# Performance work log

Hardware: AMD Instinct MI355X
Metric: run time of the kernel (lower is better)

Reference implementation:

```python
import jax, jax.numpy as jnp
import numpy as np

N_ATOMS = 131072
AEV_DIM = 1008
OUT_DIM = 2  # sum(predicted_dim) == len(predicted_properties)
ALPHA = 0.1  # CELU alpha (ANI standard)
# per-element hidden widths for ['H','C','O','N','S','F','Cl']
WIDTHS = [(256, 192, 160), (224, 192, 160), (192, 160, 128), (192, 160, 128),
          (160, 128, 96), (160, 128, 96), (160, 128, 96)]
W1MAX, W2MAX, W3MAX = 256, 192, 160


def _celu(x):
    return jax.nn.celu(x, alpha=ALPHA)


def setup_inputs() -> dict:
    key = jax.random.key(0)
    ks = jax.random.split(key, 2 + 7 * 8)
    species = jax.random.randint(ks[0], (N_ATOMS,), 0, 7)
    aev = jax.random.normal(ks[1], (N_ATOMS, AEV_DIM), dtype=jnp.float32)

    # Padded, stacked per-element weights; only the [:w] blocks are used.
    W1 = np.zeros((7, AEV_DIM, W1MAX), np.float32); b1 = np.zeros((7, W1MAX), np.float32)
    W2 = np.zeros((7, W1MAX, W2MAX), np.float32);  b2 = np.zeros((7, W2MAX), np.float32)
    W3 = np.zeros((7, W2MAX, W3MAX), np.float32);  b3 = np.zeros((7, W3MAX), np.float32)
    Wh = np.zeros((7, W3MAX, OUT_DIM), np.float32); bh = np.zeros((7, OUT_DIM), np.float32)
    for e, (w1, w2, w3) in enumerate(WIDTHS):
        kk = ks[2 + 8 * e: 2 + 8 * (e + 1)]
        W1[e, :, :w1] = np.asarray(jax.random.normal(kk[0], (AEV_DIM, w1))) / np.sqrt(AEV_DIM)
        b1[e, :w1] = np.asarray(jax.random.normal(kk[1], (w1,))) * 0.01
        W2[e, :w1, :w2] = np.asarray(jax.random.normal(kk[2], (w1, w2))) / np.sqrt(w1)
        b2[e, :w2] = np.asarray(jax.random.normal(kk[3], (w2,))) * 0.01
        W3[e, :w2, :w3] = np.asarray(jax.random.normal(kk[4], (w2, w3))) / np.sqrt(w2)
        b3[e, :w3] = np.asarray(jax.random.normal(kk[5], (w3,))) * 0.01
        Wh[e, :w3, :] = np.asarray(jax.random.normal(kk[6], (w3, OUT_DIM))) / np.sqrt(w3)
        bh[e, :] = np.asarray(jax.random.normal(kk[7], (OUT_DIM,))) * 0.01
    return {
        "species": species, "aev": aev,
        "W1": jnp.asarray(W1), "b1": jnp.asarray(b1),
        "W2": jnp.asarray(W2), "b2": jnp.asarray(b2),
        "W3": jnp.asarray(W3), "b3": jnp.asarray(b3),
        "Wh": jnp.asarray(Wh), "bh": jnp.asarray(bh),
    }


def reference(species, aev, W1, b1, W2, b2, W3, b3, Wh, bh):
    # species-routed dispatch -> per-element 3-layer MLP + 2 linear heads -> combine
    out = jnp.zeros((aev.shape[0], OUT_DIM), dtype=aev.dtype)
    for e, (w1, w2, w3) in enumerate(WIDTHS):  # fixed set of 7 structurally distinct experts
        h = _celu(aev @ W1[e, :, :w1] + b1[e, :w1])          # [N, w1]
        h = _celu(h @ W2[e, :w1, :w2] + b2[e, :w2])          # [N, w2]
        h = _celu(h @ W3[e, :w2, :w3] + b3[e, :w3])          # [N, w3]
        y = h @ Wh[e, :w3, :] + bh[e]                        # [N, 2]
        out = out + jnp.where((species == e)[:, None], y, jnp.zeros((), aev.dtype))
    return out
```

## Files before the change

kernel.cpp:

```cpp
#include <hip/hip_runtime.h>

#define NS 7
#define NA 131072
#define AEVD 1008
#define KP1 1024
#define N1 256
#define N2 192
#define N3 160

typedef __attribute__((ext_vector_type(8))) short short8;
typedef __attribute__((ext_vector_type(8))) unsigned short ushortx8;
typedef __attribute__((ext_vector_type(4))) float f32x4;
typedef __attribute__((ext_vector_type(4))) float fvec4;
typedef unsigned short u16;

#define BAR() asm volatile("s_waitcnt lgkmcnt(0)\ns_barrier" ::: "memory")

__device__ __forceinline__ u16 f2bf(float f) {
  unsigned u = __builtin_bit_cast(unsigned, f);
  u += 0x7fffu + ((u >> 16) & 1u);
  return (u16)(u >> 16);
}
__device__ __forceinline__ float bf2f(u16 h) {
  return __builtin_bit_cast(float, ((unsigned)h) << 16);
}
__device__ __forceinline__ float celu_f(float x) {
  return x > 0.f ? x : 0.1f * (__expf(x * 10.f) - 1.f);
}
__device__ __forceinline__ void pack8(fvec4 a, fvec4 b, ushortx8* dst) {
  ushortx8 p;
  p[0] = f2bf(a.x); p[1] = f2bf(a.y); p[2] = f2bf(a.z); p[3] = f2bf(a.w);
  p[4] = f2bf(b.x); p[5] = f2bf(b.y); p[6] = f2bf(b.z); p[7] = f2bf(b.w);
  *dst = p;
}
__device__ __forceinline__ fvec4 ld_aev(const float* row, int k) {
  if (k < AEVD) return *(const fvec4*)(row + k);
  fvec4 z = {0.f, 0.f, 0.f, 0.f};
  return z;
}

__global__ void count_kernel(const int* __restrict__ species, int* __restrict__ counts) {
  __shared__ int h[NS];
  if (threadIdx.x < NS) h[threadIdx.x] = 0;
  __syncthreads();
  int i = blockIdx.x * blockDim.x + threadIdx.x;
  if (i < NA) atomicAdd(&h[species[i]], 1);
  __syncthreads();
  if (threadIdx.x < NS) atomicAdd(&counts[threadIdx.x], h[threadIdx.x]);
}

__global__ void scan_kernel(const int* __restrict__ counts, int* __restrict__ offsets,
                            int* __restrict__ cursors, int* __restrict__ blockStart) {
  int off = 0, bs = 0;
  for (int e = 0; e < NS; ++e) {
    offsets[e] = off; cursors[e] = off; blockStart[e] = bs;
    off += counts[e];
    bs += (counts[e] + 63) >> 6;
  }
  offsets[NS] = off; blockStart[NS] = bs;
}

__global__ void scatter_kernel(const int* __restrict__ species, int* __restrict__ cursors,
                               int* __restrict__ idx) {
  __shared__ int h[NS], lb[NS];
  if (threadIdx.x < NS) h[threadIdx.x] = 0;
  __syncthreads();
  int i = blockIdx.x * blockDim.x + threadIdx.x;
  int s = species[i];
  int lpos = atomicAdd(&h[s], 1);
  __syncthreads();
  if (threadIdx.x < NS) lb[threadIdx.x] = atomicAdd(&cursors[threadIdx.x], h[threadIdx.x]);
  __syncthreads();
  idx[lb[s] + lpos] = i;
}

__global__ void convert_w(const float* __restrict__ src, u16* __restrict__ dst,
                          int K, int N, int KP) {
  long total = (long)NS * N * KP;
  for (long i = (long)blockIdx.x * blockDim.x + threadIdx.x; i < total;
       i += (long)gridDim.x * blockDim.x) {
    int kp = (int)(i % KP);
    long t2 = i / KP;
    int n = (int)(t2 % N);
    int e = (int)(t2 / N);
    float v = (kp < K) ? src[((long)e * K + kp) * N + n] : 0.f;
    dst[i] = f2bf(v);
  }
}

#define H1P 264
#define H2P 200
#define H3P 168

__global__ __launch_bounds__(256, 2) void ani_fused(
    const int* __restrict__ idx, const int* __restrict__ counts,
    const int* __restrict__ offsets, const int* __restrict__ blockStart,
    const float* __restrict__ aev,
    const u16* __restrict__ W1t, const float* __restrict__ b1,
    const u16* __restrict__ W2t, const float* __restrict__ b2,
    const u16* __restrict__ W3t, const float* __restrict__ b3,
    const u16* __restrict__ Wht, const float* __restrict__ bh,
    float* __restrict__ out) {
  __shared__ __align__(16) u16 AB[2][64 * 72];
  __shared__ __align__(16) u16 H1[64 * H1P];
  __shared__ __align__(16) u16 H2[64 * H2P];
  u16* H3 = H1;

  int bid = blockIdx.x;
  if (bid >= blockStart[NS]) return;
  int e = 0;
#pragma unroll
  for (int s = 1; s < NS; ++s)
    if (bid >= blockStart[s]) e = s;
  int t = bid - blockStart[e];
  int base = offsets[e] + (t << 6);
  int mcount = counts[e] - (t << 6);
  if (mcount > 64) mcount = 64;

  int tid = threadIdx.x;
  int lane = tid & 63;
  int w = tid >> 6;
  int lr = lane & 15;
  int kg = lane >> 4;

  int arow = tid >> 2;
  int aks = (tid & 3) << 4;
  int rrow = arow < mcount ? arow : (mcount - 1);
  const float* aevRow = aev + (size_t)idx[base + rrow] * AEVD;

  const u16* Wb1 = W1t + ((size_t)e * N1 + (w * 64 + lr)) * KP1 + kg * 8;

  auto loadA = [&](int chunk, fvec4 (&v)[4]) {
    int kb = chunk * 64 + aks;
    v[0] = ld_aev(aevRow, kb);
    v[1] = ld_aev(aevRow, kb + 4);
    v[2] = ld_aev(aevRow, kb + 8);
    v[3] = ld_aev(aevRow, kb + 12);
  };
  auto loadB1 = [&](int chunk, short8 (&b)[2][4]) {
#pragma unroll
    for (int kk = 0; kk < 2; ++kk)
#pragma unroll
      for (int ni = 0; ni < 4; ++ni)
        b[kk][ni] = *(const short8*)(Wb1 + (size_t)ni * 16 * KP1 + chunk * 64 + kk * 32);
  };

  f32x4 acc[4][4] = {};

  auto iter1 = [&](int c, int p, short8 (&bfr)[2][4], fvec4 (&pre)[4]) {
    short8 af[2][4];
#pragma unroll
    for (int kk = 0; kk < 2; ++kk)
#pragma unroll
      for (int mi = 0; mi < 4; ++mi)
        af[kk][mi] = *(const short8*)&AB[p][(mi * 16 + lr) * 72 + kk * 32 + kg * 8];
    if (c + 1 < 16) {
      pack8(pre[0], pre[1], (ushortx8*)&AB[p ^ 1][arow * 72 + aks]);
      pack8(pre[2], pre[3], (ushortx8*)&AB[p ^ 1][arow * 72 + aks + 8]);
    }
    if (c + 3 < 16) loadA(c + 3, pre);
#pragma unroll
    for (int kk = 0; kk < 2; ++kk)
#pragma unroll
      for (int ni = 0; ni < 4; ++ni)
#pragma unroll
        for (int mi = 0; mi < 4; ++mi)
          acc[mi][ni] = __builtin_amdgcn_mfma_f32_16x16x32_bf16(af[kk][mi], bfr[kk][ni], acc[mi][ni], 0, 0, 0);
    if (c + 2 < 16) loadB1(c + 2, bfr);
    BAR();
  };

  {
    fvec4 t0[4];
    loadA(0, t0);
    pack8(t0[0], t0[1], (ushortx8*)&AB[0][arow * 72 + aks]);
    pack8(t0[2], t0[3], (ushortx8*)&AB[0][arow * 72 + aks + 8]);
  }
  fvec4 pA[4], pB[4];
  loadA(1, pA);
  loadA(2, pB);
  short8 bA[2][4], bB[2][4];
  loadB1(0, bA);
  loadB1(1, bB);
  BAR();

  for (int c = 0; c < 16; c += 2) {
    iter1(c, 0, bA, pA);
    iter1(c + 1, 1, bB, pB);
  }

  int mr2 = (w & 1) * 32;
  int nc2 = (w >> 1) * 96;
  const u16* Wb2 = W2t + ((size_t)e * N2 + (nc2 + lr)) * N1 + kg * 8;
  auto loadB2 = [&](int k0, short8 (&b)[6]) {
#pragma unroll
    for (int ni = 0; ni < 6; ++ni)
      b[ni] = *(const short8*)(Wb2 + (size_t)ni * 16 * N1 + k0);
  };
  short8 c2A[6], c2B[6], c2C[6], c2D[6];
  loadB2(0, c2A); loadB2(32, c2B); loadB2(64, c2C); loadB2(96, c2D);

#pragma unroll
  for (int ni = 0; ni < 4; ++ni) {
    int col = w * 64 + ni * 16 + lr;
    float bias = b1[e * N1 + col];
#pragma unroll
    for (int mi = 0; mi < 4; ++mi)
#pragma unroll
      for (int r = 0; r < 4; ++r)
        H1[(mi * 16 + kg * 4 + r) * H1P + col] = f2bf(celu_f(acc[mi][ni][r] + bias));
  }
  BAR();

  f32x4 acc2[2][6] = {};
  auto mm2 = [&](int k0, short8 (&b)[6]) {
    short8 a0 = *(const short8*)&H1[(mr2 + lr) * H1P + k0 + kg * 8];
    short8 a1 = *(const short8*)&H1[(mr2 + 16 + lr) * H1P + k0 + kg * 8];
#pragma unroll
    for (int ni = 0; ni < 6; ++ni) {
      acc2[0][ni] = __builtin_amdgcn_mfma_f32_16x16x32_bf16(a0, b[ni], acc2[0][ni], 0, 0, 0);
      acc2[1][ni] = __builtin_amdgcn_mfma_f32_16x16x32_bf16(a1, b[ni], acc2[1][ni], 0, 0, 0);
    }
  };
  mm2(0, c2A);   loadB2(128, c2A);
  mm2(32, c2B);  loadB2(160, c2B);
  mm2(64, c2C);  loadB2(192, c2C);
  mm2(96, c2D);  loadB2(224, c2D);
  mm2(128, c2A);
  mm2(160, c2B);
  mm2(192, c2C);
  mm2(224, c2D);

  int mr3 = (w & 1) * 32;
  int nc3 = (w >> 1) * 80;
  const u16* Wb3 = W3t + ((size_t)e * N3 + (nc3 + lr)) * N2 + kg * 8;
  auto loadB3 = [&](int k0, short8 (&b)[5]) {
#pragma unroll
    for (int ni = 0; ni < 5; ++ni)
      b[ni] = *(const short8*)(Wb3 + (size_t)ni * 16 * N2 + k0);
  };
  short8 c3A[5], c3B[5], c3C[5];
  loadB3(0, c3A); loadB3(32, c3B); loadB3(64, c3C);

#pragma unroll
  for (int ni = 0; ni < 6; ++ni) {
    int col = nc2 + ni * 16 + lr;
    float bias = b2[e * N2 + col];
#pragma unroll
    for (int mi = 0; mi < 2; ++mi)
#pragma unroll
      for (int r = 0; r < 4; ++r)
        H2[(mr2 + mi * 16 + kg * 4 + r) * H2P + col] = f2bf(celu_f(acc2[mi][ni][r] + bias));
  }
  BAR();

  f32x4 acc3[2][5] = {};
  auto mm3 = [&](int k0, short8 (&b)[5]) {
    short8 a0 = *(const short8*)&H2[(mr3 + lr) * H2P + k0 + kg * 8];
    short8 a1 = *(const short8*)&H2[(mr3 + 16 + lr) * H2P + k0 + kg * 8];
#pragma unroll
    for (int ni = 0; ni < 5; ++ni) {
      acc3[0][ni] = __builtin_amdgcn_mfma_f32_16x16x32_bf16(a0, b[ni], acc3[0][ni], 0, 0, 0);
      acc3[1][ni] = __builtin_amdgcn_mfma_f32_16x16x32_bf16(a1, b[ni], acc3[1][ni], 0, 0, 0);
    }
  };
  mm3(0, c3A);   loadB3(96, c3A);
  mm3(32, c3B);  loadB3(128, c3B);
  mm3(64, c3C);  loadB3(160, c3C);
  mm3(96, c3A);
  mm3(128, c3B);
  mm3(160, c3C);

  int hr_ = tid >> 2;
  int ho = (tid >> 1) & 1;
  int kh = tid & 1;
  const u16* wr = Wht + ((size_t)e * 2 + ho) * N3 + kh * 80;
  ushortx8 wvv[10];
#pragma unroll
  for (int c = 0; c < 10; ++c) wvv[c] = *(const ushortx8*)&wr[c * 8];

#pragma unroll
  for (int ni = 0; ni < 5; ++ni) {
    int col = nc3 + ni * 16 + lr;
    float bias = b3[e * N3 + col];
#pragma unroll
    for (int mi = 0; mi < 2; ++mi)
#pragma unroll
      for (int r = 0; r < 4; ++r)
        H3[(mr3 + mi * 16 + kg * 4 + r) * H3P + col] = f2bf(celu_f(acc3[mi][ni][r] + bias));
  }
  BAR();

  {
    float s = 0.f;
    const u16* hrow = &H3[hr_ * H3P + kh * 80];
#pragma unroll
    for (int c = 0; c < 10; ++c) {
      ushortx8 hv = *(const ushortx8*)&hrow[c * 8];
#pragma unroll
      for (int j = 0; j < 8; ++j) s += bf2f(hv[j]) * bf2f(wvv[c][j]);
    }
    s += __shfl_xor(s, 1);
    if (kh == 0 && hr_ < mcount) out[(size_t)idx[base + hr_] * 2 + ho] = s + bh[e * 2 + ho];
  }
}

extern "C" void kernel_launch(void* const* d_in, const int* in_sizes, int n_in,
                              void* d_out, int out_size, void* d_ws, size_t ws_size,
                              hipStream_t stream) {
  const int* species = (const int*)d_in[0];
  const float* aev = (const float*)d_in[1];
  const float* W1 = (const float*)d_in[2];
  const float* b1 = (const float*)d_in[3];
  const float* W2 = (const float*)d_in[4];
  const float* b2 = (const float*)d_in[5];
  const float* W3 = (const float*)d_in[6];
  const float* b3 = (const float*)d_in[7];
  const float* Wh = (const float*)d_in[8];
  const float* bh = (const float*)d_in[9];
  float* out = (float*)d_out;

  char* p = (char*)d_ws;
  int* counts = (int*)p; p += 32;
  int* offsets = (int*)p; p += 32;
  int* cursors = (int*)p; p += 32;
  int* blockStart = (int*)p; p += 32;
  int* idx = (int*)p; p += (size_t)NA * 4;
  u16* W1t = (u16*)p; p += (size_t)NS * N1 * KP1 * 2;
  u16* W2t = (u16*)p; p += (size_t)NS * N2 * N1 * 2;
  u16* W3t = (u16*)p; p += (size_t)NS * N3 * N2 * 2;
  u16* Wht = (u16*)p; p += (size_t)NS * 2 * N3 * 2;

  (void)hipMemsetAsync(counts, 0, 32, stream);
  count_kernel<<<NA / 256, 256, 0, stream>>>(species, counts);
  scan_kernel<<<1, 1, 0, stream>>>(counts, offsets, cursors, blockStart);
  scatter_kernel<<<NA / 256, 256, 0, stream>>>(species, cursors, idx);

  convert_w<<<2048, 256, 0, stream>>>(W1, W1t, AEVD, N1, KP1);
  convert_w<<<1024, 256, 0, stream>>>(W2, W2t, N1, N2, N1);
  convert_w<<<512, 256, 0, stream>>>(W3, W3t, N2, N3, N2);
  convert_w<<<16, 256, 0, stream>>>(Wh, Wht, N3, 2, N3);

  int maxBlocks = (NA >> 6) + NS;
  ani_fused<<<maxBlocks, 256, 0, stream>>>(idx, counts, offsets, blockStart, aev,
                                           W1t, b1, W2t, b2, W3t, b3, Wht, bh, out);
}
```

Before: 328.5 us.

## Restructure layer-1 GEMM into four 256-wide K quarters with deep register prefetch

Measured after the change: 358.9 us. 1.09x slower.

```diff
diff --git a/kernel.cpp b/kernel.cpp
--- a/kernel.cpp
+++ b/kernel.cpp
@@ -10,11 +10,10 @@
 
 typedef __attribute__((ext_vector_type(8))) short short8;
 typedef __attribute__((ext_vector_type(8))) unsigned short ushortx8;
+typedef __attribute__((ext_vector_type(4))) unsigned short ushortx4;
 typedef __attribute__((ext_vector_type(4))) float f32x4;
 typedef __attribute__((ext_vector_type(4))) float fvec4;
 typedef unsigned short u16;
-
-#define BAR() asm volatile("s_waitcnt lgkmcnt(0)\ns_barrier" ::: "memory")
 
 __device__ __forceinline__ u16 f2bf(float f) {
   unsigned u = __builtin_bit_cast(unsigned, f);
@@ -26,17 +25,6 @@
 }
 __device__ __forceinline__ float celu_f(float x) {
   return x > 0.f ? x : 0.1f * (__expf(x * 10.f) - 1.f);
-}
-__device__ __forceinline__ void pack8(fvec4 a, fvec4 b, ushortx8* dst) {
-  ushortx8 p;
-  p[0] = f2bf(a.x); p[1] = f2bf(a.y); p[2] = f2bf(a.z); p[3] = f2bf(a.w);
-  p[4] = f2bf(b.x); p[5] = f2bf(b.y); p[6] = f2bf(b.z); p[7] = f2bf(b.w);
-  *dst = p;
-}
-__device__ __forceinline__ fvec4 ld_aev(const float* row, int k) {
-  if (k < AEVD) return *(const fvec4*)(row + k);
-  fvec4 z = {0.f, 0.f, 0.f, 0.f};
-  return z;
 }
 
 __global__ void count_kernel(const int* __restrict__ species, int* __restrict__ counts) {
@@ -88,7 +76,7 @@
   }
 }
 
-#define H1P 264
+#define AP 264
 #define H2P 200
 #define H3P 168
 
@@ -101,10 +89,10 @@
     const u16* __restrict__ W3t, const float* __restrict__ b3,
     const u16* __restrict__ Wht, const float* __restrict__ bh,
     float* __restrict__ out) {
-  __shared__ __align__(16) u16 AB[2][64 * 72];
-  __shared__ __align__(16) u16 H1[64 * H1P];
-  __shared__ __align__(16) u16 H2[64 * H2P];
-  u16* H3 = H1;
+  __shared__ __align__(16) u16 S[2][64 * AP];
+  u16* H1 = &S[0][0];
+  u16* H2 = &S[1][0];
+  u16* H3 = &S[0][0];
 
   int bid = blockIdx.x;
   if (bid >= blockStart[NS]) return;
@@ -124,70 +112,59 @@
   int kg = lane >> 4;
 
   int arow = tid >> 2;
-  int aks = (tid & 3) << 4;
+  int sub = tid & 3;
   int rrow = arow < mcount ? arow : (mcount - 1);
   const float* aevRow = aev + (size_t)idx[base + rrow] * AEVD;
 
   const u16* Wb1 = W1t + ((size_t)e * N1 + (w * 64 + lr)) * KP1 + kg * 8;
 
-  auto loadA = [&](int chunk, fvec4 (&v)[4]) {
-    int kb = chunk * 64 + aks;
-    v[0] = ld_aev(aevRow, kb);
-    v[1] = ld_aev(aevRow, kb + 4);
-    v[2] = ld_aev(aevRow, kb + 8);
-    v[3] = ld_aev(aevRow, kb + 12);
-  };
-  auto loadB1 = [&](int chunk, short8 (&b)[2][4]) {
-#pragma unroll
-    for (int kk = 0; kk < 2; ++kk)
+  fvec4 L[16];
+  auto loadQ = [&](int q) {
+#pragma unroll
+    for (int j = 0; j < 16; ++j) {
+      int k = q * 256 + (sub + j * 4) * 4;
+      if (k < AEVD) L[j] = *(const fvec4*)(aevRow + k);
+      else { fvec4 z = {0.f, 0.f, 0.f, 0.f}; L[j] = z; }
+    }
+  };
+  auto packQ = [&](int b) {
+#pragma unroll
+    for (int j = 0; j < 16; ++j) {
+      ushortx4 p;
+      p[0] = f2bf(L[j].x); p[1] = f2bf(L[j].y);
+      p[2] = f2bf(L[j].z); p[3] = f2bf(L[j].w);
+      *(ushortx4*)&S[b][arow * AP + (sub + j * 4) * 4] = p;
+    }
+  };
+
+  f32x4 acc[4][4] = {};
+  auto computeQ = [&](int q, int b) {
+#pragma unroll
+    for (int ks = 0; ks < 8; ++ks) {
+      short8 af[4], bf[4];
+#pragma unroll
+      for (int mi = 0; mi < 4; ++mi)
+        af[mi] = *(const short8*)&S[b][(mi * 16 + lr) * AP + ks * 32 + kg * 8];
 #pragma unroll
       for (int ni = 0; ni < 4; ++ni)
-        b[kk][ni] = *(const short8*)(Wb1 + (size_t)ni * 16 * KP1 + chunk * 64 + kk * 32);
-  };
-
-  f32x4 acc[4][4] = {};
-
-  auto iter1 = [&](int c, int p, short8 (&bfr)[2][4], fvec4 (&pre)[4]) {
-    short8 af[2][4];
-#pragma unroll
-    for (int kk = 0; kk < 2; ++kk)
-#pragma unroll
-      for (int mi = 0; mi < 4; ++mi)
-        af[kk][mi] = *(const short8*)&AB[p][(mi * 16 + lr) * 72 + kk * 32 + kg * 8];
-    if (c + 1 < 16) {
-      pack8(pre[0], pre[1], (ushortx8*)&AB[p ^ 1][arow * 72 + aks]);
-      pack8(pre[2], pre[3], (ushortx8*)&AB[p ^ 1][arow * 72 + aks + 8]);
-    }
-    if (c + 3 < 16) loadA(c + 3, pre);
-#pragma unroll
-    for (int kk = 0; kk < 2; ++kk)
+        bf[ni] = *(const short8*)(Wb1 + (size_t)ni * 16 * KP1 + q * 256 + ks * 32);
 #pragma unroll
       for (int ni = 0; ni < 4; ++ni)
 #pragma unroll
         for (int mi = 0; mi < 4; ++mi)
-          acc[mi][ni] = __builtin_amdgcn_mfma_f32_16x16x32_bf16(af[kk][mi], bfr[kk][ni], acc[mi][ni], 0, 0, 0);
-    if (c + 2 < 16) loadB1(c + 2, bfr);
-    BAR();
-  };
-
-  {
-    fvec4 t0[4];
-    loadA(0, t0);
-    pack8(t0[0], t0[1], (ushortx8*)&AB[0][arow * 72 + aks]);
-    pack8(t0[2], t0[3], (ushortx8*)&AB[0][arow * 72 + aks + 8]);
-  }
-  fvec4 pA[4], pB[4];
-  loadA(1, pA);
-  loadA(2, pB);
-  short8 bA[2][4], bB[2][4];
-  loadB1(0, bA);
-  loadB1(1, bB);
-  BAR();
-
-  for (int c = 0; c < 16; c += 2) {
-    iter1(c, 0, bA, pA);
-    iter1(c + 1, 1, bB, pB);
-  }
+          acc[mi][ni] = __builtin_amdgcn_mfma_f32_16x16x32_bf16(af[mi], bf[ni], acc[mi][ni], 0, 0, 0);
+    }
+  };
+
+  loadQ(0); packQ(0); loadQ(1);
+  __syncthreads();
+  computeQ(0, 0); packQ(1); loadQ(2);
+  __syncthreads();
+  computeQ(1, 1); packQ(0); loadQ(3);
+  __syncthreads();
+  computeQ(2, 0); packQ(1);
+  __syncthreads();
+  computeQ(3, 1);
 
   int mr2 = (w & 1) * 32;
   int nc2 = (w >> 1) * 96;
@@ -208,14 +185,14 @@
     for (int mi = 0; mi < 4; ++mi)
 #pragma unroll
       for (int r = 0; r < 4; ++r)
-        H1[(mi * 16 + kg * 4 + r) * H1P + col] = f2bf(celu_f(acc[mi][ni][r] + bias));
-  }
-  BAR();
+        H1[(mi * 16 + kg * 4 + r) * AP + col] = f2bf(celu_f(acc[mi][ni][r] + bias));
+  }
+  __syncthreads();
 
   f32x4 acc2[2][6] = {};
   auto mm2 = [&](int k0, short8 (&b)[6]) {
-    short8 a0 = *(const short8*)&H1[(mr2 + lr) * H1P + k0 + kg * 8];
-    short8 a1 = *(const short8*)&H1[(mr2 + 16 + lr) * H1P + k0 + kg * 8];
+    short8 a0 = *(const short8*)&H1[(mr2 + lr) * AP + k0 + kg * 8];
+    short8 a1 = *(const short8*)&H1[(mr2 + 16 + lr) * AP + k0 + kg * 8];
 #pragma unroll
     for (int ni = 0; ni < 6; ++ni) {
       acc2[0][ni] = __builtin_amdgcn_mfma_f32_16x16x32_bf16(a0, b[ni], acc2[0][ni], 0, 0, 0);
@@ -252,7 +229,7 @@
       for (int r = 0; r < 4; ++r)
         H2[(mr2 + mi * 16 + kg * 4 + r) * H2P + col] = f2bf(celu_f(acc2[mi][ni][r] + bias));
   }
-  BAR();
+  __syncthreads();
 
   f32x4 acc3[2][5] = {};
   auto mm3 = [&](int k0, short8 (&b)[5]) {
@@ -289,7 +266,7 @@
       for (int r = 0; r < 4; ++r)
         H3[(mr3 + mi * 16 + kg * 4 + r) * H3P + col] = f2bf(celu_f(acc3[mi][ni][r] + bias));
   }
-  BAR();
+  __syncthreads();
 
   {
     float s = 0.f;
```

## Shrink tiles to 32 atoms with 2 waves, remap blocks across XCDs

Applied to the files above, without the earlier changes.

Measured after the change: 428.7 us. 30.5% more time.

```diff
diff --git a/kernel.cpp b/kernel.cpp
--- a/kernel.cpp
+++ b/kernel.cpp
@@ -7,6 +7,11 @@
 #define N1 256
 #define N2 192
 #define N3 160
+#define GR 32
+#define APITCH 40
+#define H1P 264
+#define H2P 200
+#define H3P 168
 
 typedef __attribute__((ext_vector_type(8))) short short8;
 typedef __attribute__((ext_vector_type(8))) unsigned short ushortx8;
@@ -27,14 +32,8 @@
 __device__ __forceinline__ float celu_f(float x) {
   return x > 0.f ? x : 0.1f * (__expf(x * 10.f) - 1.f);
 }
-__device__ __forceinline__ void pack8(fvec4 a, fvec4 b, ushortx8* dst) {
-  ushortx8 p;
-  p[0] = f2bf(a.x); p[1] = f2bf(a.y); p[2] = f2bf(a.z); p[3] = f2bf(a.w);
-  p[4] = f2bf(b.x); p[5] = f2bf(b.y); p[6] = f2bf(b.z); p[7] = f2bf(b.w);
-  *dst = p;
-}
 __device__ __forceinline__ fvec4 ld_aev(const float* row, int k) {
-  if (k < AEVD) return *(const fvec4*)(row + k);
+  if (k + 4 <= AEVD) return *(const fvec4*)(row + k);
   fvec4 z = {0.f, 0.f, 0.f, 0.f};
   return z;
 }
@@ -50,14 +49,14 @@
 }
 
 __global__ void scan_kernel(const int* __restrict__ counts, int* __restrict__ offsets,
-                            int* __restrict__ cursors, int* __restrict__ blockStart) {
-  int off = 0, bs = 0;
+                            int* __restrict__ cursors, int* __restrict__ gstart) {
+  int off = 0, gs = 0;
   for (int e = 0; e < NS; ++e) {
-    offsets[e] = off; cursors[e] = off; blockStart[e] = bs;
+    offsets[e] = off; cursors[e] = off; gstart[e] = gs;
     off += counts[e];
-    bs += (counts[e] + 63) >> 6;
-  }
-  offsets[NS] = off; blockStart[NS] = bs;
+    gs += (counts[e] + GR - 1) / GR;
+  }
+  offsets[NS] = off; gstart[NS] = gs;
 }
 
 __global__ void scatter_kernel(const int* __restrict__ species, int* __restrict__ cursors,
@@ -88,34 +87,36 @@
   }
 }
 
-#define H1P 264
-#define H2P 200
-#define H3P 168
-
-__global__ __launch_bounds__(256, 2) void ani_fused(
+__global__ __launch_bounds__(128, 2) void ani_fused(
     const int* __restrict__ idx, const int* __restrict__ counts,
-    const int* __restrict__ offsets, const int* __restrict__ blockStart,
+    const int* __restrict__ offsets, const int* __restrict__ gstart,
     const float* __restrict__ aev,
     const u16* __restrict__ W1t, const float* __restrict__ b1,
     const u16* __restrict__ W2t, const float* __restrict__ b2,
     const u16* __restrict__ W3t, const float* __restrict__ b3,
     const u16* __restrict__ Wht, const float* __restrict__ bh,
     float* __restrict__ out) {
-  __shared__ __align__(16) u16 AB[2][64 * 72];
-  __shared__ __align__(16) u16 H1[64 * H1P];
-  __shared__ __align__(16) u16 H2[64 * H2P];
-  u16* H3 = H1;
-
-  int bid = blockIdx.x;
-  if (bid >= blockStart[NS]) return;
+  __shared__ __align__(16) u16 REG0[GR * H2P];
+  __shared__ __align__(16) u16 REG1[GR * H1P];
+  u16* H1 = REG1;
+  u16* H2 = REG0;
+  u16* H3 = REG1;
+
+  int gd = gridDim.x;
+  int b0 = blockIdx.x;
+  int q = gd >> 3, r = gd & 7;
+  int xcd = b0 & 7, ii = b0 >> 3;
+  int bid = (xcd < r ? xcd * (q + 1) : r * (q + 1) + (xcd - r) * q) + ii;
+
+  if (bid >= gstart[NS]) return;
   int e = 0;
 #pragma unroll
   for (int s = 1; s < NS; ++s)
-    if (bid >= blockStart[s]) e = s;
-  int t = bid - blockStart[e];
-  int base = offsets[e] + (t << 6);
-  int mcount = counts[e] - (t << 6);
-  if (mcount > 64) mcount = 64;
+    if (bid >= gstart[s]) e = s;
+  int t0 = bid - gstart[e];
+  int base = offsets[e] + t0 * GR;
+  int mcount = counts[e] - t0 * GR;
+  if (mcount > GR) mcount = GR;
 
   int tid = threadIdx.x;
   int lane = tid & 63;
@@ -124,152 +125,133 @@
   int kg = lane >> 4;
 
   int arow = tid >> 2;
-  int aks = (tid & 3) << 4;
-  int rrow = arow < mcount ? arow : (mcount - 1);
+  int koff = (tid & 3) << 3;
+  int rrow = arow < mcount ? arow : mcount - 1;
   const float* aevRow = aev + (size_t)idx[base + rrow] * AEVD;
 
-  const u16* Wb1 = W1t + ((size_t)e * N1 + (w * 64 + lr)) * KP1 + kg * 8;
-
-  auto loadA = [&](int chunk, fvec4 (&v)[4]) {
-    int kb = chunk * 64 + aks;
-    v[0] = ld_aev(aevRow, kb);
-    v[1] = ld_aev(aevRow, kb + 4);
-    v[2] = ld_aev(aevRow, kb + 8);
-    v[3] = ld_aev(aevRow, kb + 12);
-  };
-  auto loadB1 = [&](int chunk, short8 (&b)[2][4]) {
-#pragma unroll
-    for (int kk = 0; kk < 2; ++kk)
-#pragma unroll
-      for (int ni = 0; ni < 4; ++ni)
-        b[kk][ni] = *(const short8*)(Wb1 + (size_t)ni * 16 * KP1 + chunk * 64 + kk * 32);
-  };
-
-  f32x4 acc[4][4] = {};
-
-  auto iter1 = [&](int c, int p, short8 (&bfr)[2][4], fvec4 (&pre)[4]) {
-    short8 af[2][4];
-#pragma unroll
-    for (int kk = 0; kk < 2; ++kk)
-#pragma unroll
-      for (int mi = 0; mi < 4; ++mi)
-        af[kk][mi] = *(const short8*)&AB[p][(mi * 16 + lr) * 72 + kk * 32 + kg * 8];
-    if (c + 1 < 16) {
-      pack8(pre[0], pre[1], (ushortx8*)&AB[p ^ 1][arow * 72 + aks]);
-      pack8(pre[2], pre[3], (ushortx8*)&AB[p ^ 1][arow * 72 + aks + 8]);
+  const u16* Wb1 = W1t + ((size_t)e * N1 + (w * 128 + lr)) * KP1 + kg * 8;
+
+  fvec4 Ar[3][2];
+  short8 Br[2][8];
+
+  auto loadA = [&](int c, fvec4 (&d)[2]) {
+    int k = c * 32 + koff;
+    d[0] = ld_aev(aevRow, k);
+    d[1] = ld_aev(aevRow, k + 4);
+  };
+  auto packA = [&](fvec4 (&v)[2], int buf) {
+    ushortx8 p;
+    p[0] = f2bf(v[0].x); p[1] = f2bf(v[0].y); p[2] = f2bf(v[0].z); p[3] = f2bf(v[0].w);
+    p[4] = f2bf(v[1].x); p[5] = f2bf(v[1].y); p[6] = f2bf(v[1].z); p[7] = f2bf(v[1].w);
+    *(ushortx8*)&REG0[buf * GR * APITCH + arow * APITCH + koff] = p;
+  };
+  auto loadB1 = [&](int c, short8 (&d)[8]) {
+#pragma unroll
+    for (int ni = 0; ni < 8; ++ni)
+      d[ni] = *(const short8*)(Wb1 + (size_t)ni * 16 * KP1 + c * 32);
+  };
+
+  f32x4 acc[2][8] = {};
+
+  loadA(0, Ar[0]); loadA(1, Ar[1]); loadA(2, Ar[2]);
+  loadB1(0, Br[0]); loadB1(1, Br[1]);
+  packA(Ar[0], 0);
+  BAR();
+
+#pragma unroll
+  for (int c = 0; c < 32; ++c) {
+    if (c + 3 < 32) loadA(c + 3, Ar[(c + 3) % 3]);
+    short8 af0 = *(const short8*)&REG0[(c & 1) * GR * APITCH + lr * APITCH + kg * 8];
+    short8 af1 = *(const short8*)&REG0[(c & 1) * GR * APITCH + (16 + lr) * APITCH + kg * 8];
+    __builtin_amdgcn_s_setprio(1);
+#pragma unroll
+    for (int ni = 0; ni < 8; ++ni) {
+      acc[0][ni] = __builtin_amdgcn_mfma_f32_16x16x32_bf16(af0, Br[c & 1][ni], acc[0][ni], 0, 0, 0);
+      acc[1][ni] = __builtin_amdgcn_mfma_f32_16x16x32_bf16(af1, Br[c & 1][ni], acc[1][ni], 0, 0, 0);
     }
-    if (c + 3 < 16) loadA(c + 3, pre);
-#pragma unroll
-    for (int kk = 0; kk < 2; ++kk)
-#pragma unroll
-      for (int ni = 0; ni < 4; ++ni)
-#pragma unroll
-        for (int mi = 0; mi < 4; ++mi)
-          acc[mi][ni] = __builtin_amdgcn_mfma_f32_16x16x32_bf16(af[kk][mi], bfr[kk][ni], acc[mi][ni], 0, 0, 0);
-    if (c + 2 < 16) loadB1(c + 2, bfr);
+    __builtin_amdgcn_s_setprio(0);
+    if (c + 1 < 32) packA(Ar[(c + 1) % 3], (c + 1) & 1);
+    if (c + 2 < 32) loadB1(c + 2, Br[c & 1]);
     BAR();
-  };
-
-  {
-    fvec4 t0[4];
-    loadA(0, t0);
-    pack8(t0[0], t0[1], (ushortx8*)&AB[0][arow * 72 + aks]);
-    pack8(t0[2], t0[3], (ushortx8*)&AB[0][arow * 72 + aks + 8]);
-  }
-  fvec4 pA[4], pB[4];
-  loadA(1, pA);
-  loadA(2, pB);
-  short8 bA[2][4], bB[2][4];
-  loadB1(0, bA);
-  loadB1(1, bB);
+  }
+
+  const u16* Wb2 = W2t + ((size_t)e * N2 + (w * 96 + lr)) * N1 + kg * 8;
+  auto loadB2 = [&](int ks, short8 (&d)[6]) {
+#pragma unroll
+    for (int ni = 0; ni < 6; ++ni)
+      d[ni] = *(const short8*)(Wb2 + (size_t)ni * 16 * N1 + ks * 32);
+  };
+  short8 r2a[6], r2b[6];
+  loadB2(0, r2a); loadB2(1, r2b);
+
+#pragma unroll
+  for (int ni = 0; ni < 8; ++ni) {
+    int col = w * 128 + ni * 16 + lr;
+    float bias = b1[e * N1 + col];
+#pragma unroll
+    for (int mi = 0; mi < 2; ++mi)
+#pragma unroll
+      for (int rr = 0; rr < 4; ++rr)
+        H1[(mi * 16 + kg * 4 + rr) * H1P + col] = f2bf(celu_f(acc[mi][ni][rr] + bias));
+  }
   BAR();
 
-  for (int c = 0; c < 16; c += 2) {
-    iter1(c, 0, bA, pA);
-    iter1(c + 1, 1, bB, pB);
-  }
-
-  int mr2 = (w & 1) * 32;
-  int nc2 = (w >> 1) * 96;
-  const u16* Wb2 = W2t + ((size_t)e * N2 + (nc2 + lr)) * N1 + kg * 8;
-  auto loadB2 = [&](int k0, short8 (&b)[6]) {
-#pragma unroll
-    for (int ni = 0; ni < 6; ++ni)
-      b[ni] = *(const short8*)(Wb2 + (size_t)ni * 16 * N1 + k0);
-  };
-  short8 c2A[6], c2B[6], c2C[6], c2D[6];
-  loadB2(0, c2A); loadB2(32, c2B); loadB2(64, c2C); loadB2(96, c2D);
-
-#pragma unroll
-  for (int ni = 0; ni < 4; ++ni) {
-    int col = w * 64 + ni * 16 + lr;
-    float bias = b1[e * N1 + col];
-#pragma unroll
-    for (int mi = 0; mi < 4; ++mi)
-#pragma unroll
-      for (int r = 0; r < 4; ++r)
-        H1[(mi * 16 + kg * 4 + r) * H1P + col] = f2bf(celu_f(acc[mi][ni][r] + bias));
-  }
-  BAR();
-
   f32x4 acc2[2][6] = {};
-  auto mm2 = [&](int k0, short8 (&b)[6]) {
-    short8 a0 = *(const short8*)&H1[(mr2 + lr) * H1P + k0 + kg * 8];
-    short8 a1 = *(const short8*)&H1[(mr2 + 16 + lr) * H1P + k0 + kg * 8];
+  auto mm2 = [&](int ks, short8 (&b)[6]) {
+    short8 a0 = *(const short8*)&H1[lr * H1P + ks * 32 + kg * 8];
+    short8 a1 = *(const short8*)&H1[(16 + lr) * H1P + ks * 32 + kg * 8];
 #pragma unroll
     for (int ni = 0; ni < 6; ++ni) {
       acc2[0][ni] = __builtin_amdgcn_mfma_f32_16x16x32_bf16(a0, b[ni], acc2[0][ni], 0, 0, 0);
       acc2[1][ni] = __builtin_amdgcn_mfma_f32_16x16x32_bf16(a1, b[ni], acc2[1][ni], 0, 0, 0);
     }
   };
-  mm2(0, c2A);   loadB2(128, c2A);
-  mm2(32, c2B);  loadB2(160, c2B);
-  mm2(64, c2C);  loadB2(192, c2C);
-  mm2(96, c2D);  loadB2(224, c2D);
-  mm2(128, c2A);
-  mm2(160, c2B);
-  mm2(192, c2C);
-  mm2(224, c2D);
-
-  int mr3 = (w & 1) * 32;
-  int nc3 = (w >> 1) * 80;
-  const u16* Wb3 = W3t + ((size_t)e * N3 + (nc3 + lr)) * N2 + kg * 8;
-  auto loadB3 = [&](int k0, short8 (&b)[5]) {
+  mm2(0, r2a); loadB2(2, r2a);
+  mm2(1, r2b); loadB2(3, r2b);
+  mm2(2, r2a); loadB2(4, r2a);
+  mm2(3, r2b); loadB2(5, r2b);
+  mm2(4, r2a); loadB2(6, r2a);
+  mm2(5, r2b); loadB2(7, r2b);
+  mm2(6, r2a);
+  mm2(7, r2b);
+
+  const u16* Wb3 = W3t + ((size_t)e * N3 + (w * 80 + lr)) * N2 + kg * 8;
+  auto loadB3 = [&](int ks, short8 (&d)[5]) {
 #pragma unroll
     for (int ni = 0; ni < 5; ++ni)
-      b[ni] = *(const short8*)(Wb3 + (size_t)ni * 16 * N2 + k0);
-  };
-  short8 c3A[5], c3B[5], c3C[5];
-  loadB3(0, c3A); loadB3(32, c3B); loadB3(64, c3C);
+      d[ni] = *(const short8*)(Wb3 + (size_t)ni * 16 * N2 + ks * 32);
+  };
+  short8 r3a[5], r3b[5];
+  loadB3(0, r3a); loadB3(1, r3b);
 
 #pragma unroll
   for (int ni = 0; ni < 6; ++ni) {
-    int col = nc2 + ni * 16 + lr;
+    int col = w * 96 + ni * 16 + lr;
     float bias = b2[e * N2 + col];
 #pragma unroll
     for (int mi = 0; mi < 2; ++mi)
 #pragma unroll
-      for (int r = 0; r < 4; ++r)
-        H2[(mr2 + mi * 16 + kg * 4 + r) * H2P + col] = f2bf(celu_f(acc2[mi][ni][r] + bias));
+      for (int rr = 0; rr < 4; ++rr)
+        H2[(mi * 16 + kg * 4 + rr) * H2P + col] = f2bf(celu_f(acc2[mi][ni][rr] + bias));
   }
   BAR();
 
   f32x4 acc3[2][5] = {};
-  auto mm3 = [&](int k0, short8 (&b)[5]) {
-    short8 a0 = *(const short8*)&H2[(mr3 + lr) * H2P + k0 + kg * 8];
-    short8 a1 = *(const short8*)&H2[(mr3 + 16 + lr) * H2P + k0 + kg * 8];
+  auto mm3 = [&](int ks, short8 (&b)[5]) {
+    short8 a0 = *(const short8*)&H2[lr * H2P + ks * 32 + kg * 8];
+    short8 a1 = *(const short8*)&H2[(16 + lr) * H2P + ks * 32 + kg * 8];
 #pragma unroll
     for (int ni = 0; ni < 5; ++ni) {
       acc3[0][ni] = __builtin_amdgcn_mfma_f32_16x16x32_bf16(a0, b[ni], acc3[0][ni], 0, 0, 0);
       acc3[1][ni] = __builtin_amdgcn_mfma_f32_16x16x32_bf16(a1, b[ni], acc3[1][ni], 0, 0, 0);
     }
   };
-  mm3(0, c3A);   loadB3(96, c3A);
-  mm3(32, c3B);  loadB3(128, c3B);
-  mm3(64, c3C);  loadB3(160, c3C);
-  mm3(96, c3A);
-  mm3(128, c3B);
-  mm3(160, c3C);
+  mm3(0, r3a); loadB3(2, r3a);
+  mm3(1, r3b); loadB3(3, r3b);
+  mm3(2, r3a); loadB3(4, r3a);
+  mm3(3, r3b); loadB3(5, r3b);
+  mm3(4, r3a);
+  mm3(5, r3b);
 
   int hr_ = tid >> 2;
   int ho = (tid >> 1) & 1;
@@ -281,13 +263,13 @@
 
 #pragma unroll
   for (int ni = 0; ni < 5; ++ni) {
-    int col = nc3 + ni * 16 + lr;
+    int col = w * 80 + ni * 16 + lr;
     float bias = b3[e * N3 + col];
 #pragma unroll
     for (int mi = 0; mi < 2; ++mi)
 #pragma unroll
-      for (int r = 0; r < 4; ++r)
-        H3[(mr3 + mi * 16 + kg * 4 + r) * H3P + col] = f2bf(celu_f(acc3[mi][ni][r] + bias));
+      for (int rr = 0; rr < 4; ++rr)
+        H3[(mi * 16 + kg * 4 + rr) * H3P + col] = f2bf(celu_f(acc3[mi][ni][rr] + bias));
   }
   BAR();
 
@@ -324,7 +306,7 @@
   int* counts = (int*)p; p += 32;
   int* offsets = (int*)p; p += 32;
   int* cursors = (int*)p; p += 32;
-  int* blockStart = (int*)p; p += 32;
+  int* gstart = (int*)p; p += 32;
   int* idx = (int*)p; p += (size_t)NA * 4;
   u16* W1t = (u16*)p; p += (size_t)NS * N1 * KP1 * 2;
   u16* W2t = (u16*)p; p += (size_t)NS * N2 * N1 * 2;
@@ -333,7 +315,7 @@
 
   (void)hipMemsetAsync(counts, 0, 32, stream);
   count_kernel<<<NA / 256, 256, 0, stream>>>(species, counts);
-  scan_kernel<<<1, 1, 0, stream>>>(counts, offsets, cursors, blockStart);
+  scan_kernel<<<1, 1, 0, stream>>>(counts, offsets, cursors, gstart);
   scatter_kernel<<<NA / 256, 256, 0, stream>>>(species, cursors, idx);
 
   convert_w<<<2048, 256, 0, stream>>>(W1, W1t, AEVD, N1, KP1);
@@ -341,7 +323,7 @@
   convert_w<<<512, 256, 0, stream>>>(W3, W3t, N2, N3, N2);
   convert_w<<<16, 256, 0, stream>>>(Wh, Wht, N3, 2, N3);
 
-  int maxBlocks = (NA >> 6) + NS;
-  ani_fused<<<maxBlocks, 256, 0, stream>>>(idx, counts, offsets, blockStart, aev,
+  int maxBlocks = NA / GR + NS;
+  ani_fused<<<maxBlocks, 128, 0, stream>>>(idx, counts, offsets, gstart, aev,
                                            W1t, b1, W2t, b2, W3t, b3, Wht, bh, out);
 }
```
